# Performance work log

Hardware: AMD Instinct MI355X
Metric: run time of the kernel (lower is better)

## Reference

```python
import jax, jax.numpy as jnp
import numpy as np

# ---- static configuration (mirrors TimeFold init + deterministic prepare()) ----
B = 256
F = 512            # fft_length//2 + 1
T = 81             # input STFT frames
WIN = 1022         # window_length == frame_length == fft_length
HOP = 400          # hop_length
SEG = 1000         # segment_length
OVL = 50           # overlap_length
TO_HOP = 100       # deterministic choice of randint(1, hop_size=100)
SIG_LEN = (T - 1) * HOP + WIN            # 33022, inverse_stft output length

# prepare(): t segments kept, gaps of TO_HOP deleted
_t = SIG_LEN // (SEG + TO_HOP)
if SIG_LEN % (SEG + TO_HOP) >= SEG:
    _t += 1                               # _t = 30
KEPT_LEN = _t * SEG                       # 30000
OUT_LEN = SEG + (_t - 1) * (SEG - OVL)    # 28550
NF = 1 + (OUT_LEN - WIN) // HOP           # 69 output STFT frames

# indices kept after deleting the to_hop gaps (complement of delete_indices)
KEEP_IDX = np.concatenate([k * (SEG + TO_HOP) + np.arange(SEG) for k in range(_t)])

# overlap-add blending coefficients (length KEPT_LEN), built exactly as in prepare()
_ramp_up = np.arange(1, OVL + 1, dtype=np.float32) / OVL
_ramp_dn = np.arange(OVL, 0, -1, dtype=np.float32) / OVL
COEFF_INC = np.pad(np.tile(np.pad(_ramp_up, (0, SEG - OVL)), _t - 1), (SEG - OVL, OVL))
COEFF_DEC = np.pad(np.tile(np.pad(_ramp_dn, (SEG - OVL, 0)), _t - 1), (0, SEG))
_c = np.tile(np.pad(np.ones(SEG - 2 * OVL, np.float32), (OVL, OVL)), _t - 2)
_c = np.pad(np.pad(_c, (OVL, 0)), (SEG - OVL, 0), constant_values=1.0)
_c = np.pad(np.pad(_c, (0, OVL)), (0, SEG - OVL), constant_values=1.0)
COEFF_CONST = _c.astype(np.float32)

# final_delete_indices: drop [k*SEG, k*SEG+OVL) for k = 1.._t-1
_mask = np.ones(KEPT_LEN, bool)
for k in range(1, _t):
    _mask[k * SEG:k * SEG + OVL] = False
FINAL_KEEP = np.nonzero(_mask)[0]         # length OUT_LEN

# gather index grids for framing (static)
ISTFT_IDX = np.arange(T)[:, None] * HOP + np.arange(WIN)[None, :]
STFT_IDX = np.arange(NF)[:, None] * HOP + np.arange(WIN)[None, :]


def _hann(n):
    # periodic Hann, matches tf.signal.hann_window(periodic=True)
    return (0.5 - 0.5 * jnp.cos(2.0 * jnp.pi * jnp.arange(n, dtype=jnp.float32) / n)).astype(jnp.float32)


def _synthesis_window():
    w = _hann(WIN)
    denom = w * w
    overlaps = -(-WIN // HOP)
    denom = jnp.pad(denom, (0, overlaps * HOP - WIN))
    denom = denom.reshape(overlaps, HOP).sum(axis=0)
    denom = jnp.tile(denom, overlaps)[:WIN]
    return w / denom


def setup_inputs() -> dict:
    key = jax.random.key(0)
    x = jax.random.normal(key, (B, F, T, 2), dtype=jnp.float32)
    return {"x": x}


def reference(x) -> jnp.ndarray:
    # x: [B, 512, T, 2] real/imag STFT
    stfts = jax.lax.complex(x[..., 0], x[..., 1])          # [B, F, T]
    frames = jnp.transpose(stfts, (0, 2, 1))               # [B, T, F]
    # inverse_stft: irfft each frame, apply synthesis window, overlap-add
    tf_frames = jnp.fft.irfft(frames, n=WIN, axis=-1)
    tf_frames = tf_frames * _synthesis_window()
    sig = jnp.zeros((x.shape[0], SIG_LEN), jnp.float32).at[:, ISTFT_IDX].add(tf_frames)
    # dynamic segment delete (gather of kept indices)
    kept = sig[:, KEEP_IDX]                                # [B, KEPT_LEN]
    # shifted copy: drop first OVL samples, zero-pad at end
    shifted = jnp.concatenate(
        [kept[:, OVL:], jnp.zeros((x.shape[0], OVL), jnp.float32)], axis=1)
    # weighted overlap-add blend
    out = (jnp.asarray(COEFF_CONST) + jnp.asarray(COEFF_DEC)) * kept \
        + jnp.asarray(COEFF_INC) * shifted
    out = out[:, FINAL_KEEP]                               # [B, OUT_LEN]
    # forward STFT (periodic Hann, no padding)
    fr = out[:, STFT_IDX] * _hann(WIN)
    S = jnp.fft.rfft(fr, n=WIN, axis=-1)                   # [B, NF, 512]
    S = jnp.transpose(S, (0, 2, 1))                        # [B, 512, NF]
    return jnp.stack([S.real, S.imag], axis=-1)            # [B, 512, NF, 2]
```

## Files before the change

kernel.cpp:

```cpp
#include <hip/hip_runtime.h>
#include <math.h>

typedef unsigned short u16;
typedef unsigned int u32;

#define B_   256
#define F_   512
#define T_   81
#define WIN_ 1022
#define HOP_ 400
#define NF_  69
#define OUT_LEN_ 28550
#define SEG_ 1000
#define OVL_ 50

#define MA_  20736
#define MB_  17664
#define K_   1024
#define NMA_TILES 162
#define NMB_TILES 138
#define NMA_PAD   168
#define NMB_PAD   144

#define BASA_B     0u
#define BASB_B     (BASA_B + 2097152u)
#define ABUF_B     (BASB_B + 2097152u)
#define TF_B       (ABUF_B + 42467328u)
#define OUTF_B     (TF_B + 42467328u)
#define OUTF_STRIDE_ 28672

typedef __attribute__((ext_vector_type(8))) short bf8_t;
typedef __attribute__((ext_vector_type(4))) float f4_t;
typedef const __attribute__((address_space(1))) void* as1cv;
typedef __attribute__((address_space(3))) void* as3v;

__device__ __forceinline__ float b2f(u16 v) {
  u32 u = ((u32)v) << 16; float f; __builtin_memcpy(&f, &u, 4); return f;
}
__device__ __forceinline__ u16 f2b(float f) {
  u32 u; __builtin_memcpy(&u, &f, 4);
  return (u16)((u + 0x7fffu + ((u >> 16) & 1u)) >> 16);
}

__global__ __launch_bounds__(256) void gen_basisA(u16* __restrict__ BA) {
  int n = blockIdx.x;
  const float twopi_N = 6.283185307179586f / (float)WIN_;
  float scale = 0.f;
  if (n < WIN_) {
    float w = 0.5f - 0.5f * cosf(twopi_N * (float)n);
    int j = n % HOP_;
    float a = 0.5f - 0.5f * cosf(twopi_N * (float)j);
    float b = 0.5f - 0.5f * cosf(twopi_N * (float)(j + 400));
    float d = a * a + b * b;
    if (j + 800 < WIN_) {
      float c2 = 0.5f - 0.5f * cosf(twopi_N * (float)(j + 800));
      d += c2 * c2;
    }
    scale = (w / d) * (1.0f / (float)WIN_);
  }
  for (int k = threadIdx.x; k < 512; k += 256) {
    int m = (k * n) % WIN_;
    float ang = twopi_N * (float)m;
    float s, c; __sincosf(ang, &s, &c);
    bool edge = (k == 0) || (k == 511);
    float ck = edge ? 1.f : 2.f;
    float re = scale * ck * c;
    float im = edge ? 0.f : -scale * ck * s;
    BA[(size_t)n * K_ + 2 * k]     = f2b(re);
    BA[(size_t)n * K_ + 2 * k + 1] = f2b(im);
  }
}

__global__ __launch_bounds__(256) void gen_basisB(u16* __restrict__ BB) {
  int k = blockIdx.x;
  const float twopi_N = 6.283185307179586f / (float)WIN_;
  for (int w = threadIdx.x; w < K_; w += 256) {
    float re = 0.f, im = 0.f;
    if (w < WIN_) {
      int m = (k * w) % WIN_;
      float ang = twopi_N * (float)m;
      float s, c; __sincosf(ang, &s, &c);
      float h = 0.5f - 0.5f * cosf(twopi_N * (float)w);
      re = h * c; im = -h * s;
    }
    BB[(size_t)(2 * k)     * K_ + w] = f2b(re);
    BB[(size_t)(2 * k + 1) * K_ + w] = f2b(im);
  }
}

__global__ __launch_bounds__(256) void prep1(const float* __restrict__ x,
                                             u16* __restrict__ Abuf) {
  __shared__ float2 tile[32][33];
  int k0 = blockIdx.x * 32, t0 = blockIdx.y * 32, b = blockIdx.z;
  int c = threadIdx.x & 31, rr = threadIdx.x >> 5;
  const float2* xp = (const float2*)x;
#pragma unroll
  for (int i = 0; i < 4; ++i) {
    int k = k0 + rr + 8 * i, t = t0 + c;
    float2 v = make_float2(0.f, 0.f);
    if (t < T_) v = xp[(size_t)(b * F_ + k) * T_ + t];
    tile[rr + 8 * i][c] = v;
  }
  __syncthreads();
#pragma unroll
  for (int i = 0; i < 4; ++i) {
    int t = t0 + rr + 8 * i, kc = c;
    if (t < T_) {
      float2 v = tile[kc][rr + 8 * i];
      u32 packed = (u32)f2b(v.x) | ((u32)f2b(v.y) << 16);
      *(u32*)&Abuf[(size_t)(b * T_ + t) * K_ + 2 * (k0 + kc)] = packed;
    }
  }
}

template <int EPI>
__global__ __launch_bounds__(256) void gemm_bf16(const u16* __restrict__ A,
                                                 const u16* __restrict__ Bt,
                                                 void* __restrict__ Cout) {
  __shared__ u16 sA[2][4096];
  __shared__ u16 sB[2][4096];
  const int tid = threadIdx.x;
  const int lane = tid & 63, wv = tid >> 6;

  int id = blockIdx.x;
  int xcd = id & 7, slot = id >> 3;
  int mt = (slot >> 3) * 8 + xcd;
  int nt = slot & 7;
  const int nM = (EPI == 0) ? NMA_TILES : NMB_TILES;
  if (mt >= nM) return;
  const int bm = mt * 128, bn = nt * 128;

  const int fr = lane & 15, fq = lane >> 4;
  const int s0 = 2 * wv, s1 = s0 + 1;

  const u16 *pA0, *pA1;
  if (EPI == 0) {
    pA0 = A + (size_t)(bm + 16 * s0 + fr) * K_ + fq * 8;
    pA1 = A + (size_t)(bm + 16 * s1 + fr) * K_ + fq * 8;
  } else {
    int m0 = bm + 16 * s0 + fr;
    int b0 = m0 / NF_, f0 = m0 - b0 * NF_;
    pA0 = A + (size_t)b0 * OUTF_STRIDE_ + f0 * HOP_ + fq * 8;
    int m1 = m0 + 16;
    int b1 = m1 / NF_, f1 = m1 - b1 * NF_;
    pA1 = A + (size_t)b1 * OUTF_STRIDE_ + f1 * HOP_ + fq * 8;
  }
  const u16* pB0 = Bt + (size_t)(bn + 16 * s0 + fr) * K_ + fq * 8;
  const u16* pB1 = Bt + (size_t)(bn + 16 * s1 + fr) * K_ + fq * 8;

  f4_t acc[4][4];
#pragma unroll
  for (int i = 0; i < 4; ++i)
#pragma unroll
    for (int j = 0; j < 4; ++j) acc[i][j] = (f4_t){0.f, 0.f, 0.f, 0.f};

  const int wm4 = (wv >> 1) * 4, wn4 = (wv & 1) * 4;

  __builtin_amdgcn_global_load_lds((as1cv)(const void*)pA0, (as3v)(sA[0] + s0 * 512), 16, 0, 0);
  __builtin_amdgcn_global_load_lds((as1cv)(const void*)pA1, (as3v)(sA[0] + s1 * 512), 16, 0, 0);
  __builtin_amdgcn_global_load_lds((as1cv)(const void*)pB0, (as3v)(sB[0] + s0 * 512), 16, 0, 0);
  __builtin_amdgcn_global_load_lds((as1cv)(const void*)pB1, (as3v)(sB[0] + s1 * 512), 16, 0, 0);
  __builtin_amdgcn_s_waitcnt(0x0f70);
  __syncthreads();

  int cur = 0;
  for (int k0 = 0; k0 < K_; k0 += 32) {
    int nxt = k0 + 32;
    if (nxt < K_) {
      u16* dA = sA[cur ^ 1];
      u16* dB = sB[cur ^ 1];
      __builtin_amdgcn_global_load_lds((as1cv)(const void*)(pA0 + nxt), (as3v)(dA + s0 * 512), 16, 0, 0);
      __builtin_amdgcn_global_load_lds((as1cv)(const void*)(pA1 + nxt), (as3v)(dA + s1 * 512), 16, 0, 0);
      __builtin_amdgcn_global_load_lds((as1cv)(const void*)(pB0 + nxt), (as3v)(dB + s0 * 512), 16, 0, 0);
      __builtin_amdgcn_global_load_lds((as1cv)(const void*)(pB1 + nxt), (as3v)(dB + s1 * 512), 16, 0, 0);
    }

    const u16* cA = sA[cur];
    const u16* cB = sB[cur];
    bf8_t af[4], bq[4];
#pragma unroll
    for (int i = 0; i < 4; ++i)
      af[i] = *(const bf8_t*)&cA[(wm4 + i) * 512 + lane * 8];
#pragma unroll
    for (int j = 0; j < 4; ++j)
      bq[j] = *(const bf8_t*)&cB[(wn4 + j) * 512 + lane * 8];
#pragma unroll
    for (int i = 0; i < 4; ++i)
#pragma unroll
      for (int j = 0; j < 4; ++j)
        acc[i][j] = __builtin_amdgcn_mfma_f32_16x16x32_bf16(af[i], bq[j], acc[i][j], 0, 0, 0);

    __syncthreads();
    cur ^= 1;
  }

  const int wm = wm4 * 16, wn = wn4 * 16;
  if (EPI == 0) {
    u16* C = (u16*)Cout;
#pragma unroll
    for (int i = 0; i < 4; ++i)
#pragma unroll
      for (int j = 0; j < 4; ++j) {
        int colg = bn + wn + 16 * j + fr;
#pragma unroll
        for (int r = 0; r < 4; ++r) {
          int rowg = bm + wm + 16 * i + fq * 4 + r;
          C[(size_t)rowg * K_ + colg] = f2b(acc[i][j][r]);
        }
      }
  } else {
    float* out = (float*)Cout;
    float* ep = ((wv & 2) ? (float*)sB[0] : (float*)sA[0]) + (wv & 1) * 1024;
    for (int j = 0; j < 4; ++j) {
#pragma unroll
      for (int i = 0; i < 4; ++i)
#pragma unroll
        for (int r = 0; r < 4; ++r) {
          int row64 = 16 * i + fq * 4 + r;
          ep[row64 * 16 + fr] = acc[i][j][r];
        }
      __syncthreads();
      int m = bm + wm + lane;
      int b = m / NF_;
      int f = m - b * NF_;
      int colbase = bn + wn + 16 * j;
#pragma unroll
      for (int a = 0; a < 8; ++a) {
        int k = (colbase >> 1) + a;
        float2 v = make_float2(ep[lane * 16 + 2 * a], ep[lane * 16 + 2 * a + 1]);
        ((float2*)out)[((size_t)b * F_ + k) * NF_ + f] = v;
      }
      __syncthreads();
    }
  }
}

__device__ __forceinline__ float sigval(const u16* __restrict__ tfb, int i) {
  int t1 = i / HOP_; if (t1 > T_ - 1) t1 = T_ - 1;
  int t0 = (i >= WIN_) ? (i - (WIN_ - 1) + HOP_ - 1) / HOP_ : 0;
  float acc = 0.f;
  for (int t = t0; t <= t1; ++t)
    acc += b2f(tfb[(size_t)t * K_ + (i - t * HOP_)]);
  return acc;
}

__global__ __launch_bounds__(256) void k3_fold(const u16* __restrict__ tf,
                                               u16* __restrict__ outf) {
  int id = blockIdx.x * 256 + threadIdx.x;
  if (id >= B_ * OUT_LEN_) return;
  int b = id / OUT_LEN_;
  int p = id - b * OUT_LEN_;
  int s, r;
  if (p < SEG_) { s = 0; r = p; }
  else {
    int q = p - SEG_;
    s = q / (SEG_ - OVL_) + 1;
    r = OVL_ + (q - (s - 1) * (SEG_ - OVL_));
  }
  const u16* tfb = tf + (size_t)b * T_ * K_;
  float val;
  if (r >= SEG_ - OVL_ && s <= 28) {
    float dec = (float)(SEG_ - r) * (1.f / (float)OVL_);
    float inc = (float)(r - (SEG_ - OVL_ - 1)) * (1.f / (float)OVL_);
    float v1 = sigval(tfb, s * 1100 + r);
    float v2 = sigval(tfb, (s + 1) * 1100 + (r - (SEG_ - OVL_)));
    val = dec * v1 + inc * v2;
  } else {
    val = sigval(tfb, s * 1100 + r);
  }
  outf[(size_t)b * OUTF_STRIDE_ + p] = f2b(val);
}

extern "C" void kernel_launch(void* const* d_in, const int* in_sizes, int n_in,
                              void* d_out, int out_size, void* d_ws, size_t ws_size,
                              hipStream_t stream) {
  const float* x = (const float*)d_in[0];
  char* ws = (char*)d_ws;
  u16* BA   = (u16*)(ws + BASA_B);
  u16* BB   = (u16*)(ws + BASB_B);
  u16* Abuf = (u16*)(ws + ABUF_B);
  u16* TF   = (u16*)(ws + TF_B);
  u16* outf = (u16*)(ws + OUTF_B);

  hipLaunchKernelGGL(gen_basisA, dim3(1024), dim3(256), 0, stream, BA);
  hipLaunchKernelGGL(gen_basisB, dim3(512), dim3(256), 0, stream, BB);
  hipLaunchKernelGGL(prep1, dim3(16, 3, 256), dim3(256), 0, stream, x, Abuf);
  hipLaunchKernelGGL((gemm_bf16<0>), dim3(NMA_PAD * 8), dim3(256), 0, stream,
                     Abuf, BA, (void*)TF);
  int n3 = B_ * OUT_LEN_;
  hipLaunchKernelGGL(k3_fold, dim3((n3 + 255) / 256), dim3(256), 0, stream, TF, outf);
  hipLaunchKernelGGL((gemm_bf16<1>), dim3(NMB_PAD * 8), dim3(256), 0, stream,
                     outf, BB, (void*)d_out);
}
```

Measured before the change: 331.4 us.

## Restructure bf16 GEMMs to 256x128 tiles with 8 waves and triple-buffered loads

Both DFT-as-GEMM kernels now use 512-thread blocks covering 256x128 output tiles, with a three-stage LDS ring that keeps two k-slices in flight. Barriers use explicit vmcnt waits, and the MFMA block runs at raised wave priority. The XCD-aware tile mapping becomes a chunked mapping with no padded grid. The epilogue drops its per-j barriers because each wave now owns a private LDS scratch region. The aim is to hide global-load latency and raise MFMA utilisation, at the cost of more LDS per block and possibly lower occupancy.

```diff
diff --git a/kernel.cpp b/kernel.cpp
--- a/kernel.cpp
+++ b/kernel.cpp
@@ -17,10 +17,8 @@
 #define MA_  20736
 #define MB_  17664
 #define K_   1024
-#define NMA_TILES 162
-#define NMB_TILES 138
-#define NMA_PAD   168
-#define NMB_PAD   144
+#define NMT_A 81
+#define NMT_B 69
 
 #define BASA_B     0u
 #define BASB_B     (BASA_B + 2097152u)
@@ -114,39 +112,35 @@
 }
 
 template <int EPI>
-__global__ __launch_bounds__(256) void gemm_bf16(const u16* __restrict__ A,
-                                                 const u16* __restrict__ Bt,
-                                                 void* __restrict__ Cout) {
-  __shared__ u16 sA[2][4096];
-  __shared__ u16 sB[2][4096];
+__global__ __launch_bounds__(512, 4) void gemm_bf16(const u16* __restrict__ A,
+                                                    const u16* __restrict__ Bt,
+                                                    void* __restrict__ Cout) {
+  __shared__ u16 sA[3][8192];
+  __shared__ u16 sB[3][4096];
   const int tid = threadIdx.x;
   const int lane = tid & 63, wv = tid >> 6;
-
+  const int wm = wv >> 1, wn = wv & 1;
+  const int fr = lane & 15, fq = lane >> 4;
+
+  const int chunk = (EPI == 0) ? NMT_A : NMT_B;
   int id = blockIdx.x;
-  int xcd = id & 7, slot = id >> 3;
-  int mt = (slot >> 3) * 8 + xcd;
-  int nt = slot & 7;
-  const int nM = (EPI == 0) ? NMA_TILES : NMB_TILES;
-  if (mt >= nM) return;
-  const int bm = mt * 128, bn = nt * 128;
-
-  const int fr = lane & 15, fq = lane >> 4;
-  const int s0 = 2 * wv, s1 = s0 + 1;
+  int wgid = (id & 7) * chunk + (id >> 3);
+  const int mt = wgid >> 3, nt = wgid & 7;
+  const int bm = mt * 256, bn = nt * 128;
 
   const u16 *pA0, *pA1;
   if (EPI == 0) {
-    pA0 = A + (size_t)(bm + 16 * s0 + fr) * K_ + fq * 8;
-    pA1 = A + (size_t)(bm + 16 * s1 + fr) * K_ + fq * 8;
+    pA0 = A + (size_t)(bm + 16 * wv + fr) * K_ + fq * 8;
+    pA1 = A + (size_t)(bm + 16 * (wv + 8) + fr) * K_ + fq * 8;
   } else {
-    int m0 = bm + 16 * s0 + fr;
+    int m0 = bm + 16 * wv + fr;
     int b0 = m0 / NF_, f0 = m0 - b0 * NF_;
     pA0 = A + (size_t)b0 * OUTF_STRIDE_ + f0 * HOP_ + fq * 8;
-    int m1 = m0 + 16;
+    int m1 = m0 + 128;
     int b1 = m1 / NF_, f1 = m1 - b1 * NF_;
     pA1 = A + (size_t)b1 * OUTF_STRIDE_ + f1 * HOP_ + fq * 8;
   }
-  const u16* pB0 = Bt + (size_t)(bn + 16 * s0 + fr) * K_ + fq * 8;
-  const u16* pB1 = Bt + (size_t)(bn + 16 * s1 + fr) * K_ + fq * 8;
+  const u16* pB0 = Bt + (size_t)(bn + 16 * wv + fr) * K_ + fq * 8;
 
   f4_t acc[4][4];
 #pragma unroll
@@ -154,63 +148,71 @@
 #pragma unroll
     for (int j = 0; j < 4; ++j) acc[i][j] = (f4_t){0.f, 0.f, 0.f, 0.f};
 
-  const int wm4 = (wv >> 1) * 4, wn4 = (wv & 1) * 4;
-
-  __builtin_amdgcn_global_load_lds((as1cv)(const void*)pA0, (as3v)(sA[0] + s0 * 512), 16, 0, 0);
-  __builtin_amdgcn_global_load_lds((as1cv)(const void*)pA1, (as3v)(sA[0] + s1 * 512), 16, 0, 0);
-  __builtin_amdgcn_global_load_lds((as1cv)(const void*)pB0, (as3v)(sB[0] + s0 * 512), 16, 0, 0);
-  __builtin_amdgcn_global_load_lds((as1cv)(const void*)pB1, (as3v)(sB[0] + s1 * 512), 16, 0, 0);
-  __builtin_amdgcn_s_waitcnt(0x0f70);
-  __syncthreads();
-
-  int cur = 0;
-  for (int k0 = 0; k0 < K_; k0 += 32) {
-    int nxt = k0 + 32;
-    if (nxt < K_) {
-      u16* dA = sA[cur ^ 1];
-      u16* dB = sB[cur ^ 1];
-      __builtin_amdgcn_global_load_lds((as1cv)(const void*)(pA0 + nxt), (as3v)(dA + s0 * 512), 16, 0, 0);
-      __builtin_amdgcn_global_load_lds((as1cv)(const void*)(pA1 + nxt), (as3v)(dA + s1 * 512), 16, 0, 0);
-      __builtin_amdgcn_global_load_lds((as1cv)(const void*)(pB0 + nxt), (as3v)(dB + s0 * 512), 16, 0, 0);
-      __builtin_amdgcn_global_load_lds((as1cv)(const void*)(pB1 + nxt), (as3v)(dB + s1 * 512), 16, 0, 0);
-    }
-
-    const u16* cA = sA[cur];
-    const u16* cB = sB[cur];
-    bf8_t af[4], bq[4];
+  auto STAGE = [&](int t) {
+    const int buf = t % 3;
+    const int ko = t * 32;
+    __builtin_amdgcn_global_load_lds((as1cv)(const void*)(pA0 + ko),
+                                     (as3v)(&sA[buf][(wv)     * 512]), 16, 0, 0);
+    __builtin_amdgcn_global_load_lds((as1cv)(const void*)(pA1 + ko),
+                                     (as3v)(&sA[buf][(wv + 8) * 512]), 16, 0, 0);
+    __builtin_amdgcn_global_load_lds((as1cv)(const void*)(pB0 + ko),
+                                     (as3v)(&sB[buf][(wv)     * 512]), 16, 0, 0);
+  };
+
+  STAGE(0);
+  STAGE(1);
+  asm volatile("s_waitcnt vmcnt(3)" ::: "memory");
+  __builtin_amdgcn_s_barrier();
+
+#pragma unroll
+  for (int t = 0; t < 32; ++t) {
+    const int buf = t % 3;
+    bf8_t a[4], b[4];
 #pragma unroll
     for (int i = 0; i < 4; ++i)
-      af[i] = *(const bf8_t*)&cA[(wm4 + i) * 512 + lane * 8];
+      a[i] = *(const bf8_t*)&sA[buf][(wm * 4 + i) * 512 + lane * 8];
 #pragma unroll
     for (int j = 0; j < 4; ++j)
-      bq[j] = *(const bf8_t*)&cB[(wn4 + j) * 512 + lane * 8];
+      b[j] = *(const bf8_t*)&sB[buf][(wn * 4 + j) * 512 + lane * 8];
+
+    if (t + 2 < 32) STAGE(t + 2);
+
+    __builtin_amdgcn_s_setprio(1);
 #pragma unroll
     for (int i = 0; i < 4; ++i)
 #pragma unroll
       for (int j = 0; j < 4; ++j)
-        acc[i][j] = __builtin_amdgcn_mfma_f32_16x16x32_bf16(af[i], bq[j], acc[i][j], 0, 0, 0);
-
-    __syncthreads();
-    cur ^= 1;
-  }
-
-  const int wm = wm4 * 16, wn = wn4 * 16;
+        acc[i][j] = __builtin_amdgcn_mfma_f32_16x16x32_bf16(a[i], b[j], acc[i][j], 0, 0, 0);
+    __builtin_amdgcn_s_setprio(0);
+
+    if (t + 1 < 32) {
+      if (t + 2 < 32) asm volatile("s_waitcnt vmcnt(3) lgkmcnt(0)" ::: "memory");
+      else            asm volatile("s_waitcnt vmcnt(0) lgkmcnt(0)" ::: "memory");
+      __builtin_amdgcn_s_barrier();
+    }
+  }
+
+  const int wmr = wm * 64, wnc = wn * 64;
   if (EPI == 0) {
     u16* C = (u16*)Cout;
 #pragma unroll
     for (int i = 0; i < 4; ++i)
 #pragma unroll
       for (int j = 0; j < 4; ++j) {
-        int colg = bn + wn + 16 * j + fr;
+        int colg = bn + wnc + 16 * j + fr;
 #pragma unroll
         for (int r = 0; r < 4; ++r) {
-          int rowg = bm + wm + 16 * i + fq * 4 + r;
+          int rowg = bm + wmr + 16 * i + fq * 4 + r;
           C[(size_t)rowg * K_ + colg] = f2b(acc[i][j][r]);
         }
       }
   } else {
     float* out = (float*)Cout;
-    float* ep = ((wv & 2) ? (float*)sB[0] : (float*)sA[0]) + (wv & 1) * 1024;
+    __syncthreads();
+    float* ep = (float*)((char*)&sA[0][0] + wv * 4096);
+    int m = bm + wmr + lane;
+    int b = m / NF_;
+    int f = m - b * NF_;
     for (int j = 0; j < 4; ++j) {
 #pragma unroll
       for (int i = 0; i < 4; ++i)
@@ -219,18 +221,13 @@
           int row64 = 16 * i + fq * 4 + r;
           ep[row64 * 16 + fr] = acc[i][j][r];
         }
-      __syncthreads();
-      int m = bm + wm + lane;
-      int b = m / NF_;
-      int f = m - b * NF_;
-      int colbase = bn + wn + 16 * j;
-#pragma unroll
-      for (int a = 0; a < 8; ++a) {
-        int k = (colbase >> 1) + a;
-        float2 v = make_float2(ep[lane * 16 + 2 * a], ep[lane * 16 + 2 * a + 1]);
+      int colbase = bn + wnc + 16 * j;
+#pragma unroll
+      for (int a2 = 0; a2 < 8; ++a2) {
+        int k = (colbase >> 1) + a2;
+        float2 v = make_float2(ep[lane * 16 + 2 * a2], ep[lane * 16 + 2 * a2 + 1]);
         ((float2*)out)[((size_t)b * F_ + k) * NF_ + f] = v;
       }
-      __syncthreads();
     }
   }
 }
@@ -285,10 +282,10 @@
   hipLaunchKernelGGL(gen_basisA, dim3(1024), dim3(256), 0, stream, BA);
   hipLaunchKernelGGL(gen_basisB, dim3(512), dim3(256), 0, stream, BB);
   hipLaunchKernelGGL(prep1, dim3(16, 3, 256), dim3(256), 0, stream, x, Abuf);
-  hipLaunchKernelGGL((gemm_bf16<0>), dim3(NMA_PAD * 8), dim3(256), 0, stream,
+  hipLaunchKernelGGL((gemm_bf16<0>), dim3(NMT_A * 8), dim3(512), 0, stream,
                      Abuf, BA, (void*)TF);
   int n3 = B_ * OUT_LEN_;
   hipLaunchKernelGGL(k3_fold, dim3((n3 + 255) / 256), dim3(256), 0, stream, TF, outf);
-  hipLaunchKernelGGL((gemm_bf16<1>), dim3(NMB_PAD * 8), dim3(256), 0, stream,
+  hipLaunchKernelGGL((gemm_bf16<1>), dim3(NMT_B * 8), dim3(512), 0, stream,
                      outf, BB, (void*)d_out);
 }
```

After: 313.2 us. 5.5% less time.
